# Kernel tuning notes

Measured on AMD Instinct MI355X. Metric: run time of the kernel, lower is better.

The kernel has to match this reference:

```python
import jax, jax.numpy as jnp
import numpy as np

D_MODEL = 1024
HEADS = 16
DH = D_MODEL // HEADS
ROPE_THETA = 10000.0


def _rope_cache(T, dh, base, dtype):
    half = dh // 2
    inv_freq = 1.0 / (base ** (jnp.arange(half, dtype=dtype) / half))
    t = jnp.arange(T, dtype=dtype)
    freqs = jnp.outer(t, inv_freq)  # [T, half]
    return jnp.sin(freqs), jnp.cos(freqs)


def _apply_rope(x, sin, cos):
    # x: [B, h, T, dh]; sin/cos: [T, dh//2] broadcast over B,h
    half = sin.shape[-1]
    x1, x2 = x[..., :half], x[..., half:2 * half]
    return jnp.concatenate([x1 * cos - x2 * sin, x1 * sin + x2 * cos], axis=-1)


def setup_inputs() -> dict:
    key = jax.random.key(0)
    ks = jax.random.split(key, 5)
    B, T, D = 4, 2048, D_MODEL
    scale = 1.0 / np.sqrt(D)
    x_btd = jax.random.normal(ks[0], (B, T, D), dtype=jnp.float32)
    Wqkv = jax.random.normal(ks[1], (D, 3 * D), dtype=jnp.float32) * scale
    bqkv = jnp.zeros((3 * D,), dtype=jnp.float32)
    Wproj = jax.random.normal(ks[2], (D, D), dtype=jnp.float32) * scale
    bproj = jnp.zeros((D,), dtype=jnp.float32)
    return {"x_btd": x_btd, "Wqkv": Wqkv, "bqkv": bqkv, "Wproj": Wproj, "bproj": bproj}


def reference(x_btd, Wqkv, bqkv, Wproj, bproj):
    B, T, D = x_btd.shape
    h, dh = HEADS, DH
    qkv = x_btd @ Wqkv + bqkv                      # [B, T, 3D]
    q, k, v = jnp.split(qkv, 3, axis=-1)

    def to_heads(z):
        return z.reshape(B, T, h, dh).transpose(0, 2, 1, 3)  # [B, h, T, dh]

    qh, kh, vh = to_heads(q), to_heads(k), to_heads(v)
    sin, cos = _rope_cache(T, dh, ROPE_THETA, x_btd.dtype)
    qh = _apply_rope(qh, sin, cos)
    kh = _apply_rope(kh, sin, cos)

    scores = jnp.einsum('bhqd,bhkd->bhqk', qh, kh) / jnp.sqrt(jnp.asarray(dh, x_btd.dtype))
    attn = jax.nn.softmax(scores, axis=-1)
    out = jnp.einsum('bhqk,bhkd->bhqd', attn, vh)  # [B, h, T, dh]
    out = out.transpose(0, 2, 1, 3).reshape(B, T, D)
    return out @ Wproj + bproj
```

## Files before the change

kernel.cpp:

```cpp
#include <hip/hip_runtime.h>
#include <stdint.h>


typedef float  f32x4  __attribute__((ext_vector_type(4)));
typedef float  f32x16 __attribute__((ext_vector_type(16)));
typedef short  s16x8  __attribute__((ext_vector_type(8)));
typedef unsigned int u32x4 __attribute__((ext_vector_type(4)));
typedef unsigned short u16;
typedef unsigned int   u32;

#define LOG2E 1.4426950408889634f

__device__ __forceinline__ u16 f2bf(float f) {
  u32 u = __float_as_uint(f);
  u32 r = (u + 0x7fffu + ((u >> 16) & 1u)) >> 16;
  return (u16)r;
}

__device__ __forceinline__ u32 cvtpk_bf16(float lo, float hi) {
  u32 w;
  asm("v_cvt_pk_bf16_f32 %0, %1, %2" : "=v"(w) : "v"(lo), "v"(hi));
  return w;
}

__device__ __forceinline__ float fexp2(float x) {
  return __builtin_amdgcn_exp2f(x);
}

__device__ __forceinline__ void gload_lds16(const u16* g, u16* l) {
  __builtin_amdgcn_global_load_lds(
      (const __attribute__((address_space(1))) uint32_t*)g,
      (__attribute__((address_space(3))) uint32_t*)l, 16, 0, 0);
}

__global__ void rope_table_kernel(float* __restrict__ rsin, float* __restrict__ rcos) {
  int idx = blockIdx.x * 256 + threadIdx.x;
  int t = idx >> 5, i = idx & 31;
  float invf = 1.0f / powf(10000.0f, (float)i * (1.0f / 32.0f));
  float ang = (float)t * invf;
  rsin[idx] = sinf(ang);
  rcos[idx] = cosf(ang);
}

__global__ void cvt_bf16_kernel(const float* __restrict__ in, u16* __restrict__ out) {
  int i = blockIdx.x * 256 + threadIdx.x;
  const float4* p = reinterpret_cast<const float4*>(in) + (size_t)i * 2;
  float4 a = p[0], b = p[1];
  u32 w0 = (u32)f2bf(a.x) | ((u32)f2bf(a.y) << 16);
  u32 w1 = (u32)f2bf(a.z) | ((u32)f2bf(a.w) << 16);
  u32 w2 = (u32)f2bf(b.x) | ((u32)f2bf(b.y) << 16);
  u32 w3 = (u32)f2bf(b.z) | ((u32)f2bf(b.w) << 16);
  reinterpret_cast<uint4*>(out)[i] = make_uint4(w0, w1, w2, w3);
}

__global__ void transpose_cvt_kernel(const float* __restrict__ W, u16* __restrict__ Wt,
                                     int rows , int cols ) {
  __shared__ float tile[32][33];
  int k0 = blockIdx.y * 32, n0 = blockIdx.x * 32;
  int t = threadIdx.x;
  int c = t & 31, r0 = t >> 5;
  #pragma unroll
  for (int i = 0; i < 4; i++) {
    int r = r0 + i * 8;
    tile[r][c] = W[(size_t)(k0 + r) * cols + n0 + c];
  }
  __syncthreads();
  int kk = t & 31, nn0 = t >> 5;
  #pragma unroll
  for (int i = 0; i < 4; i++) {
    int nn = nn0 + i * 8;
    Wt[(size_t)(n0 + nn) * rows + k0 + kk] = f2bf(tile[kk][nn]);
  }
}

__device__ __forceinline__ void qkv_scatter_frag(
    int wavecol, int rbase, int l15, f32x4* accm ,
    const float* bias, const float* rsin, const float* rcos,
    u16* Qg, u16* Kg, u16* Vtg)
{
  int sec = wavecol >> 10;
  int h = (wavecol & 1023) >> 6;
  if (sec < 2) {
    u16* G = (sec == 0) ? Qg : Kg;
    float qs = (sec == 0) ? 0.125f * LOG2E : 1.0f;
    #pragma unroll
    for (int fc = 0; fc < 2; fc++) {
      int dh = fc * 16 + l15;
      float b1 = bias[wavecol + fc * 16 + l15];
      float b2 = bias[wavecol + fc * 16 + l15 + 32];
      #pragma unroll
      for (int j = 0; j < 4; j++) {
        int grow = rbase + j;
        int bidx = grow >> 11, tt = grow & 2047;
        float sn = rsin[tt * 32 + dh], cs = rcos[tt * 32 + dh];
        float v1 = accm[fc][j] + b1;
        float v2 = accm[fc + 2][j] + b2;
        float lo = (v1 * cs - v2 * sn) * qs;
        float hi = (v1 * sn + v2 * cs) * qs;
        size_t base = ((size_t)(bidx * 16 + h) * 2048 + tt) * 64;
        G[base + dh]      = f2bf(lo);
        G[base + dh + 32] = f2bf(hi);
      }
    }
  } else {
    #pragma unroll
    for (int fc = 0; fc < 4; fc++) {
      int dh = fc * 16 + l15;
      float bb = bias[wavecol + fc * 16 + l15];
      #pragma unroll
      for (int j = 0; j < 4; j++) {
        int grow = rbase + j;
        int bidx = grow >> 11, tt = grow & 2047;
        Vtg[((size_t)(bidx * 16 + h) * 64 + dh) * 2048 + tt] = f2bf(accm[fc][j] + bb);
      }
    }
  }
}

template<int MODE>
__global__ __launch_bounds__(256) void gemm_kernel(
    const u16* __restrict__ A, const u16* __restrict__ Bt,
    const float* __restrict__ bias,
    const float* __restrict__ rsin, const float* __restrict__ rcos,
    u16* __restrict__ Qg, u16* __restrict__ Kg, u16* __restrict__ Vtg,
    float* __restrict__ Cout, int K)
{
  __shared__ alignas(16) u16 As[128][64];
  __shared__ alignas(16) u16 Bs[128][64];
  int tid = threadIdx.x;
  int lane = tid & 63, wid = tid >> 6;
  int wr = wid >> 1, wc = wid & 1;
  int l15 = lane & 15, lg = lane >> 4;
  int row0 = blockIdx.x * 128, col0 = blockIdx.y * 128;

  f32x4 acc[4][4] = {};

  int sr = lane >> 3, sc = lane & 7;
  int scol = (sc ^ sr) * 8;
  const u16* asrc = A  + (size_t)(row0 + wid * 32 + sr) * K + scol;
  const u16* bsrc = Bt + (size_t)(col0 + wid * 32 + sr) * K + scol;
  u16* aLds = &As[0][0] + wid * 2048;
  u16* bLds = &Bs[0][0] + wid * 2048;

  for (int k0 = 0; k0 < K; k0 += 64) {
    #pragma unroll
    for (int i = 0; i < 4; i++) {
      gload_lds16(asrc + (size_t)(i * 8) * K + k0, aLds + i * 512);
      gload_lds16(bsrc + (size_t)(i * 8) * K + k0, bLds + i * 512);
    }
    __syncthreads();
    #pragma unroll
    for (int kk = 0; kk < 2; kk++) {
      s16x8 af[4], bf[4];
      #pragma unroll
      for (int m = 0; m < 4; m++) {
        int row = wr * 64 + m * 16 + l15;
        int slot = (kk * 4 + lg) ^ (l15 & 7);
        af[m] = *reinterpret_cast<const s16x8*>(&As[row][slot * 8]);
      }
      #pragma unroll
      for (int n = 0; n < 4; n++) {
        int row = wc * 64 + n * 16 + l15;
        int slot = (kk * 4 + lg) ^ (l15 & 7);
        bf[n] = *reinterpret_cast<const s16x8*>(&Bs[row][slot * 8]);
      }
      #pragma unroll
      for (int m = 0; m < 4; m++)
        #pragma unroll
        for (int n = 0; n < 4; n++)
          acc[m][n] = __builtin_amdgcn_mfma_f32_16x16x32_bf16(af[m], bf[n], acc[m][n], 0, 0, 0);
    }
    __syncthreads();
  }

  if (MODE == 0) {
    int wavecol = col0 + wc * 64;
    #pragma unroll
    for (int m = 0; m < 4; m++) {
      int rbase = row0 + wr * 64 + m * 16 + lg * 4;
      qkv_scatter_frag(wavecol, rbase, l15, acc[m], bias, rsin, rcos, Qg, Kg, Vtg);
    }
  } else {
    #pragma unroll
    for (int m = 0; m < 4; m++) {
      int grow = row0 + wr * 64 + m * 16 + lg * 4;
      #pragma unroll
      for (int fc = 0; fc < 4; fc++) {
        int col = col0 + wc * 64 + fc * 16 + l15;
        float bb = bias[col];
        #pragma unroll
        for (int j = 0; j < 4; j++)
          Cout[(size_t)(grow + j) * 1024 + col] = acc[m][fc][j] + bb;
      }
    }
  }
}

template<int MODE>
__global__ __launch_bounds__(512, 2) void gemm8_kernel(
    const u16* __restrict__ A, const u16* __restrict__ Bt,
    const float* __restrict__ bias,
    const float* __restrict__ rsin, const float* __restrict__ rcos,
    u16* __restrict__ Qg, u16* __restrict__ Kg, u16* __restrict__ Vtg,
    float* __restrict__ Cout, int K)
{
  extern __shared__ u16 lds[];
  int tid = threadIdx.x;
  int lane = tid & 63, wid = tid >> 6;
  int wr = wid >> 2, wc = wid & 3;
  int l15 = lane & 15, lg = lane >> 4;
  int row0 = blockIdx.x * 128, col0 = blockIdx.y * 256;

  f32x4 acc[4][4] = {};

  int sr = lane >> 3, sc = lane & 7;
  int scol = (sc ^ sr) * 8;
  const u16* asrc = A  + (size_t)(row0 + wid * 16 + sr) * K + scol;
  const u16* bsrc = Bt + (size_t)(col0 + wid * 32 + sr) * K + scol;

  #pragma unroll
  for (int i = 0; i < 2; i++)
    gload_lds16(asrc + (size_t)(i * 8) * K, lds + wid * 1024 + i * 512);
  #pragma unroll
  for (int i = 0; i < 4; i++)
    gload_lds16(bsrc + (size_t)(i * 8) * K, lds + 8192 + wid * 2048 + i * 512);
  #pragma unroll
  for (int i = 0; i < 2; i++)
    gload_lds16(asrc + (size_t)(i * 8) * K + 64, lds + 24576 + wid * 1024 + i * 512);
  #pragma unroll
  for (int i = 0; i < 4; i++)
    gload_lds16(bsrc + (size_t)(i * 8) * K + 64, lds + 24576 + 8192 + wid * 2048 + i * 512);
  asm volatile("s_waitcnt vmcnt(6)");
  __builtin_amdgcn_s_barrier();

  const int nt = K >> 6;
  int cur = 0;
  for (int g = 0; g < nt; ++g) {
    const u16* aB = lds + cur * 24576;
    const u16* bB = aB + 8192;
    int nxt = cur + 2; if (nxt >= 3) nxt -= 3;
    u16* aD = lds + nxt * 24576 + wid * 1024;
    u16* bD = lds + nxt * 24576 + 8192 + wid * 2048;
    size_t kn2 = (size_t)(g + 2) << 6;
    bool pre = (g + 2 < nt);

    s16x8 bf[4];
    #pragma unroll
    for (int p = 0; p < 4; p++) {
      const int kk = p >> 1, mh = p & 1;
      const int slotx = (kk * 4 + lg);
      s16x8 af[2];
      #pragma unroll
      for (int mi = 0; mi < 2; mi++) {
        int row = wr * 64 + (mh * 2 + mi) * 16 + l15;
        int slot = slotx ^ (l15 & 7);
        af[mi] = *reinterpret_cast<const s16x8*>(aB + row * 64 + slot * 8);
      }
      if (mh == 0) {
        #pragma unroll
        for (int n = 0; n < 4; n++) {
          int row = wc * 64 + n * 16 + l15;
          int slot = slotx ^ (l15 & 7);
          bf[n] = *reinterpret_cast<const s16x8*>(bB + row * 64 + slot * 8);
        }
      }
      if (p == 0 && pre) {
        #pragma unroll
        for (int i = 0; i < 2; i++)
          gload_lds16(asrc + (size_t)(i * 8) * K + kn2, aD + i * 512);
        #pragma unroll
        for (int i = 0; i < 4; i++)
          gload_lds16(bsrc + (size_t)(i * 8) * K + kn2, bD + i * 512);
      }
      __builtin_amdgcn_s_barrier();
      __builtin_amdgcn_s_setprio(1);
      #pragma unroll
      for (int mi = 0; mi < 2; mi++)
        #pragma unroll
        for (int n = 0; n < 4; n++)
          acc[mh * 2 + mi][n] =
              __builtin_amdgcn_mfma_f32_16x16x32_bf16(af[mi], bf[n], acc[mh * 2 + mi][n], 0, 0, 0);
      __builtin_amdgcn_s_setprio(0);
      __builtin_amdgcn_s_barrier();
    }
    if (pre) {
      asm volatile("s_waitcnt vmcnt(6)");
      __builtin_amdgcn_s_barrier();
    } else if (g + 1 < nt) {
      asm volatile("s_waitcnt vmcnt(0)");
      __builtin_amdgcn_s_barrier();
    }
    cur += 1; if (cur >= 3) cur -= 3;
  }

  if (MODE == 0) {
    int wavecol = col0 + wc * 64;
    #pragma unroll
    for (int m = 0; m < 4; m++) {
      int rbase = row0 + wr * 64 + m * 16 + lg * 4;
      qkv_scatter_frag(wavecol, rbase, l15, acc[m], bias, rsin, rcos, Qg, Kg, Vtg);
    }
  } else {
    #pragma unroll
    for (int m = 0; m < 4; m++) {
      int grow = row0 + wr * 64 + m * 16 + lg * 4;
      #pragma unroll
      for (int fc = 0; fc < 4; fc++) {
        int col = col0 + wc * 64 + fc * 16 + l15;
        float bb = bias[col];
        #pragma unroll
        for (int j = 0; j < 4; j++)
          Cout[(size_t)(grow + j) * 1024 + col] = acc[m][fc][j] + bb;
      }
    }
  }
}

__global__ __launch_bounds__(256, 4) void attn_kernel(
    const u16* __restrict__ Qg, const u16* __restrict__ Kg, const u16* __restrict__ Vtg,
    u16* __restrict__ Og)
{
  __shared__ alignas(16) u16 Ks[2][4096];
  __shared__ alignas(16) u16 Vs[2][4096];
  int tid = threadIdx.x;
  int lane = tid & 63, wid = tid >> 6;
  int l31 = lane & 31, hi = lane >> 5;
  int bh = blockIdx.x & 63, qt = blockIdx.x >> 6;
  int q = qt * 128 + wid * 32 + l31;
  size_t bh2048 = (size_t)bh * 2048;

  s16x8 aq[4];
  #pragma unroll
  for (int kc = 0; kc < 4; kc++)
    aq[kc] = *reinterpret_cast<const s16x8*>(Qg + (bh2048 + q) * 64 + kc * 16 + hi * 8);

  f32x16 o0 = {}, o1 = {};
  float l_run = 0.f;

  int sr = lane >> 3, sc = lane & 7;
  int scol = (sc ^ sr) * 8;
  const u16* kg0 = Kg  + (bh2048 + wid * 16 + sr) * 64 + scol;
  const u16* kg1 = kg0 + 8 * 64;
  const u16* vg0 = Vtg + ((size_t)bh * 64 + wid * 16 + sr) * 2048 + scol;
  const u16* vg1 = vg0 + 8 * 2048;
  int sdst = wid * 1024;

  int offs[2][4];
  #pragma unroll
  for (int c = 0; c < 2; c++)
    #pragma unroll
    for (int j = 0; j < 4; j++)
      offs[c][j] = (c * 32 + l31) * 64 + (((j * 2 + hi) ^ (l31 & 7)) * 8);

#define STAGE(TT, BUF) do { \
    gload_lds16(kg0 + (size_t)(TT) * 4096, &Ks[BUF][sdst]); \
    gload_lds16(kg1 + (size_t)(TT) * 4096, &Ks[BUF][sdst + 512]); \
    gload_lds16(vg0 + (size_t)(TT) * 64,   &Vs[BUF][sdst]); \
    gload_lds16(vg1 + (size_t)(TT) * 64,   &Vs[BUF][sdst + 512]); \
  } while (0)

#define COMPUTE(B) do { \
    const u16* kb = &Ks[B][0]; \
    const u16* vb = &Vs[B][0]; \
    f32x16 s0 = {}, s1 = {}; \
    __builtin_amdgcn_s_setprio(1); \
    _Pragma("unroll") \
    for (int j = 0; j < 4; j++) { \
      s16x8 kf0 = *reinterpret_cast<const s16x8*>(kb + offs[0][j]); \
      s16x8 kf1 = *reinterpret_cast<const s16x8*>(kb + offs[1][j]); \
      s0 = __builtin_amdgcn_mfma_f32_32x32x16_bf16(kf0, aq[j], s0, 0, 0, 0); \
      s1 = __builtin_amdgcn_mfma_f32_32x32x16_bf16(kf1, aq[j], s1, 0, 0, 0); \
    } \
    __builtin_amdgcn_s_setprio(0); \
    _Pragma("unroll") \
    for (int i = 0; i < 16; i++) { \
      s0[i] = fexp2(s0[i]); \
      s1[i] = fexp2(s1[i]); \
    } \
    float r0 = 0.f, r1 = 0.f, r2 = 0.f, r3 = 0.f; \
    _Pragma("unroll") \
    for (int i = 0; i < 4; i++) { \
      r0 += s0[i] + s0[i + 8]; \
      r1 += s0[i + 4] + s0[i + 12]; \
      r2 += s1[i] + s1[i + 8]; \
      r3 += s1[i + 4] + s1[i + 12]; \
    } \
    float rs = (r0 + r1) + (r2 + r3); \
    rs += __shfl_xor(rs, 32); \
    l_run += rs; \
    s16x8 pf[4]; \
    _Pragma("unroll") \
    for (int ks = 0; ks < 2; ks++) { \
      int rr = ks * 8; \
      u32 a0 = cvtpk_bf16(s0[rr + 0], s0[rr + 1]); \
      u32 b0 = cvtpk_bf16(s0[rr + 4], s0[rr + 5]); \
      u32 a1 = cvtpk_bf16(s0[rr + 2], s0[rr + 3]); \
      u32 b1 = cvtpk_bf16(s0[rr + 6], s0[rr + 7]); \
      asm volatile("v_permlane32_swap_b32 %0, %1" : "+v"(a0), "+v"(b0)); \
      asm volatile("v_permlane32_swap_b32 %0, %1" : "+v"(a1), "+v"(b1)); \
      u32x4 w = {a0, a1, b0, b1}; \
      pf[ks] = __builtin_bit_cast(s16x8, w); \
    } \
    _Pragma("unroll") \
    for (int ks = 0; ks < 2; ks++) { \
      int rr = ks * 8; \
      u32 a0 = cvtpk_bf16(s1[rr + 0], s1[rr + 1]); \
      u32 b0 = cvtpk_bf16(s1[rr + 4], s1[rr + 5]); \
      u32 a1 = cvtpk_bf16(s1[rr + 2], s1[rr + 3]); \
      u32 b1 = cvtpk_bf16(s1[rr + 6], s1[rr + 7]); \
      asm volatile("v_permlane32_swap_b32 %0, %1" : "+v"(a0), "+v"(b0)); \
      asm volatile("v_permlane32_swap_b32 %0, %1" : "+v"(a1), "+v"(b1)); \
      u32x4 w = {a0, a1, b0, b1}; \
      pf[ks + 2] = __builtin_bit_cast(s16x8, w); \
    } \
    __builtin_amdgcn_s_setprio(1); \
    _Pragma("unroll") \
    for (int ks = 0; ks < 4; ks++) { \
      s16x8 vf = *reinterpret_cast<const s16x8*>(vb + offs[0][ks]); \
      o0 = __builtin_amdgcn_mfma_f32_32x32x16_bf16(vf, pf[ks], o0, 0, 0, 0); \
    } \
    _Pragma("unroll") \
    for (int ks = 0; ks < 4; ks++) { \
      s16x8 vf = *reinterpret_cast<const s16x8*>(vb + offs[1][ks]); \
      o1 = __builtin_amdgcn_mfma_f32_32x32x16_bf16(vf, pf[ks], o1, 0, 0, 0); \
    } \
    __builtin_amdgcn_s_setprio(0); \
  } while (0)

  STAGE(0, 0);
  __syncthreads();

  for (int it = 0; it < 16; it++) {
    STAGE(2 * it + 1, 1);
    COMPUTE(0);
    __syncthreads();
    if (it < 15) STAGE(2 * it + 2, 0);
    COMPUTE(1);
    __syncthreads();
  }
#undef STAGE
#undef COMPUTE

  float inv = 1.0f / l_run;
  int b = bh >> 4, h = bh & 15;
  size_t rowbase = ((size_t)b * 2048 + q) * 1024 + h * 64;
  #pragma unroll
  for (int c2 = 0; c2 < 2; c2++) {
    #pragma unroll
    for (int g = 0; g < 4; g++) {
      float e0 = (c2 ? o1[g * 4 + 0] : o0[g * 4 + 0]) * inv;
      float e1 = (c2 ? o1[g * 4 + 1] : o0[g * 4 + 1]) * inv;
      float e2 = (c2 ? o1[g * 4 + 2] : o0[g * 4 + 2]) * inv;
      float e3 = (c2 ? o1[g * 4 + 3] : o0[g * 4 + 3]) * inv;
      u32 w0 = cvtpk_bf16(e0, e1);
      u32 w1 = cvtpk_bf16(e2, e3);
      int d = c2 * 32 + g * 8 + hi * 4;
      uint2 val; val.x = w0; val.y = w1;
      *reinterpret_cast<uint2*>(Og + rowbase + d) = val;
    }
  }
}

extern "C" void kernel_launch(void* const* d_in, const int* in_sizes, int n_in,
                              void* d_out, int out_size, void* d_ws, size_t ws_size,
                              hipStream_t stream) {
  const float* x     = (const float*)d_in[0];
  const float* Wqkv  = (const float*)d_in[1];
  const float* bqkv  = (const float*)d_in[2];
  const float* Wproj = (const float*)d_in[3];
  const float* bproj = (const float*)d_in[4];
  float* out = (float*)d_out;

  char* ws = (char*)d_ws;
  size_t off = 0;
  auto alloc = [&](size_t bytes) {
    void* p = ws + off;
    off += (bytes + 255) & ~(size_t)255;
    return p;
  };
  float* rsin  = (float*)alloc((size_t)2048 * 32 * 4);
  float* rcos  = (float*)alloc((size_t)2048 * 32 * 4);
  u16* xb      = (u16*)alloc((size_t)8192 * 1024 * 2);
  u16* Wqkvt   = (u16*)alloc((size_t)3072 * 1024 * 2);
  u16* Wprojt  = (u16*)alloc((size_t)1024 * 1024 * 2);
  u16* Qg      = (u16*)alloc((size_t)64 * 2048 * 64 * 2);
  u16* Kg      = (u16*)alloc((size_t)64 * 2048 * 64 * 2);
  u16* Vtg     = (u16*)alloc((size_t)64 * 2048 * 64 * 2);
  u16* AOg     = (u16*)alloc((size_t)8192 * 1024 * 2);

  rope_table_kernel<<<256, 256, 0, stream>>>(rsin, rcos);
  cvt_bf16_kernel<<<4096, 256, 0, stream>>>(x, xb);
  transpose_cvt_kernel<<<dim3(96, 32), 256, 0, stream>>>(Wqkv, Wqkvt, 1024, 3072);
  transpose_cvt_kernel<<<dim3(32, 32), 256, 0, stream>>>(Wproj, Wprojt, 1024, 1024);

  hipError_t ok0 = hipFuncSetAttribute(
      reinterpret_cast<const void*>(&gemm8_kernel<0>),
      hipFuncAttributeMaxDynamicSharedMemorySize, 147456);
  hipError_t ok1 = hipFuncSetAttribute(
      reinterpret_cast<const void*>(&gemm8_kernel<1>),
      hipFuncAttributeMaxDynamicSharedMemorySize, 147456);

  if (ok0 == hipSuccess) {
    gemm8_kernel<0><<<dim3(64, 12), 512, 147456, stream>>>(
        xb, Wqkvt, bqkv, rsin, rcos, Qg, Kg, Vtg, nullptr, 1024);
  } else {
    gemm_kernel<0><<<dim3(64, 24), 256, 0, stream>>>(
        xb, Wqkvt, bqkv, rsin, rcos, Qg, Kg, Vtg, nullptr, 1024);
  }

  attn_kernel<<<1024, 256, 0, stream>>>(Qg, Kg, Vtg, AOg);

  if (ok1 == hipSuccess) {
    gemm8_kernel<1><<<dim3(64, 4), 512, 147456, stream>>>(
        AOg, Wprojt, bproj, nullptr, nullptr, nullptr, nullptr, nullptr, out, 1024);
  } else {
    gemm_kernel<1><<<dim3(64, 8), 256, 0, stream>>>(
        AOg, Wprojt, bproj, nullptr, nullptr, nullptr, nullptr, nullptr, out, 1024);
  }
}
```

Before: 199.4 us.

## Process two query tiles per wave in attention and merge prep kernels

Each attention wave now handles 64 query rows (two 32-row sub-tiles) instead of 32. K and V fragments read from LDS are shared by both sub-tiles, and the grid is halved to 512 blocks with launch bounds loosened to 2 blocks per CU. Separately, the rope-table, x conversion and two weight transpose kernels are merged into one prep kernel that dispatches on block index, saving three launches. The trade-off is higher register pressure and fewer blocks, which lowers occupancy and latency hiding.

Measured after the change: 258.0 us. 29.4% more time.

```diff
diff --git a/kernel.cpp b/kernel.cpp
--- a/kernel.cpp
+++ b/kernel.cpp
@@ -33,43 +33,54 @@
       (__attribute__((address_space(3))) uint32_t*)l, 16, 0, 0);
 }
 
-__global__ void rope_table_kernel(float* __restrict__ rsin, float* __restrict__ rcos) {
-  int idx = blockIdx.x * 256 + threadIdx.x;
-  int t = idx >> 5, i = idx & 31;
-  float invf = 1.0f / powf(10000.0f, (float)i * (1.0f / 32.0f));
-  float ang = (float)t * invf;
-  rsin[idx] = sinf(ang);
-  rcos[idx] = cosf(ang);
-}
-
-__global__ void cvt_bf16_kernel(const float* __restrict__ in, u16* __restrict__ out) {
-  int i = blockIdx.x * 256 + threadIdx.x;
-  const float4* p = reinterpret_cast<const float4*>(in) + (size_t)i * 2;
-  float4 a = p[0], b = p[1];
-  u32 w0 = (u32)f2bf(a.x) | ((u32)f2bf(a.y) << 16);
-  u32 w1 = (u32)f2bf(a.z) | ((u32)f2bf(a.w) << 16);
-  u32 w2 = (u32)f2bf(b.x) | ((u32)f2bf(b.y) << 16);
-  u32 w3 = (u32)f2bf(b.z) | ((u32)f2bf(b.w) << 16);
-  reinterpret_cast<uint4*>(out)[i] = make_uint4(w0, w1, w2, w3);
-}
-
-__global__ void transpose_cvt_kernel(const float* __restrict__ W, u16* __restrict__ Wt,
-                                     int rows , int cols ) {
-  __shared__ float tile[32][33];
-  int k0 = blockIdx.y * 32, n0 = blockIdx.x * 32;
-  int t = threadIdx.x;
+__device__ __forceinline__ void transpose_body(
+    const float* __restrict__ W, u16* __restrict__ Wt,
+    int rows, int cols, int bx, int by, int t, float* tile )
+{
+  int k0 = by * 32, n0 = bx * 32;
   int c = t & 31, r0 = t >> 5;
   #pragma unroll
   for (int i = 0; i < 4; i++) {
     int r = r0 + i * 8;
-    tile[r][c] = W[(size_t)(k0 + r) * cols + n0 + c];
+    tile[r * 33 + c] = W[(size_t)(k0 + r) * cols + n0 + c];
   }
   __syncthreads();
   int kk = t & 31, nn0 = t >> 5;
   #pragma unroll
   for (int i = 0; i < 4; i++) {
     int nn = nn0 + i * 8;
-    Wt[(size_t)(n0 + nn) * rows + k0 + kk] = f2bf(tile[kk][nn]);
+    Wt[(size_t)(n0 + nn) * rows + k0 + kk] = f2bf(tile[kk * 33 + nn]);
+  }
+}
+
+__global__ void prep_kernel(const float* __restrict__ x, u16* __restrict__ xb,
+                            const float* __restrict__ Wqkv, u16* __restrict__ Wqkvt,
+                            const float* __restrict__ Wproj, u16* __restrict__ Wprojt,
+                            float* __restrict__ rsin, float* __restrict__ rcos) {
+  __shared__ float tile[32 * 33];
+  int bid = blockIdx.x, t = threadIdx.x;
+  if (bid < 4096) {
+    int i = bid * 256 + t;
+    const float4* p = reinterpret_cast<const float4*>(x) + (size_t)i * 2;
+    float4 a = p[0], b = p[1];
+    u32 w0 = (u32)f2bf(a.x) | ((u32)f2bf(a.y) << 16);
+    u32 w1 = (u32)f2bf(a.z) | ((u32)f2bf(a.w) << 16);
+    u32 w2 = (u32)f2bf(b.x) | ((u32)f2bf(b.y) << 16);
+    u32 w3 = (u32)f2bf(b.z) | ((u32)f2bf(b.w) << 16);
+    reinterpret_cast<uint4*>(xb)[i] = make_uint4(w0, w1, w2, w3);
+  } else if (bid < 4096 + 3072) {
+    int bb = bid - 4096;
+    transpose_body(Wqkv, Wqkvt, 1024, 3072, bb % 96, bb / 96, t, tile);
+  } else if (bid < 4096 + 3072 + 1024) {
+    int bb = bid - 7168;
+    transpose_body(Wproj, Wprojt, 1024, 1024, bb % 32, bb / 32, t, tile);
+  } else {
+    int idx = (bid - 8192) * 256 + t;
+    int tt = idx >> 5, i = idx & 31;
+    float invf = 1.0f / powf(10000.0f, (float)i * (1.0f / 32.0f));
+    float ang = (float)tt * invf;
+    rsin[idx] = sinf(ang);
+    rcos[idx] = cosf(ang);
   }
 }
 
@@ -316,7 +327,7 @@
   }
 }
 
-__global__ __launch_bounds__(256, 4) void attn_kernel(
+__global__ __launch_bounds__(256, 2) void attn_kernel(
     const u16* __restrict__ Qg, const u16* __restrict__ Kg, const u16* __restrict__ Vtg,
     u16* __restrict__ Og)
 {
@@ -326,16 +337,18 @@
   int lane = tid & 63, wid = tid >> 6;
   int l31 = lane & 31, hi = lane >> 5;
   int bh = blockIdx.x & 63, qt = blockIdx.x >> 6;
-  int q = qt * 128 + wid * 32 + l31;
+  int q = qt * 256 + wid * 64 + l31;
   size_t bh2048 = (size_t)bh * 2048;
 
-  s16x8 aq[4];
-  #pragma unroll
-  for (int kc = 0; kc < 4; kc++)
-    aq[kc] = *reinterpret_cast<const s16x8*>(Qg + (bh2048 + q) * 64 + kc * 16 + hi * 8);
-
-  f32x16 o0 = {}, o1 = {};
-  float l_run = 0.f;
+  s16x8 aqA[4], aqB[4];
+  #pragma unroll
+  for (int kc = 0; kc < 4; kc++) {
+    aqA[kc] = *reinterpret_cast<const s16x8*>(Qg + (bh2048 + q) * 64 + kc * 16 + hi * 8);
+    aqB[kc] = *reinterpret_cast<const s16x8*>(Qg + (bh2048 + q + 32) * 64 + kc * 16 + hi * 8);
+  }
+
+  f32x16 oA0 = {}, oA1 = {}, oB0 = {}, oB1 = {};
+  float lA = 0.f, lB = 0.f;
 
   int sr = lane >> 3, sc = lane & 7;
   int scol = (sc ^ sr) * 8;
@@ -359,19 +372,7 @@
     gload_lds16(vg1 + (size_t)(TT) * 64,   &Vs[BUF][sdst + 512]); \
   } while (0)
 
-#define COMPUTE(B) do { \
-    const u16* kb = &Ks[B][0]; \
-    const u16* vb = &Vs[B][0]; \
-    f32x16 s0 = {}, s1 = {}; \
-    __builtin_amdgcn_s_setprio(1); \
-    _Pragma("unroll") \
-    for (int j = 0; j < 4; j++) { \
-      s16x8 kf0 = *reinterpret_cast<const s16x8*>(kb + offs[0][j]); \
-      s16x8 kf1 = *reinterpret_cast<const s16x8*>(kb + offs[1][j]); \
-      s0 = __builtin_amdgcn_mfma_f32_32x32x16_bf16(kf0, aq[j], s0, 0, 0, 0); \
-      s1 = __builtin_amdgcn_mfma_f32_32x32x16_bf16(kf1, aq[j], s1, 0, 0, 0); \
-    } \
-    __builtin_amdgcn_s_setprio(0); \
+#define SOFTPACK(s0, s1, lrun, pf) do { \
     _Pragma("unroll") \
     for (int i = 0; i < 16; i++) { \
       s0[i] = fexp2(s0[i]); \
@@ -387,8 +388,7 @@
     } \
     float rs = (r0 + r1) + (r2 + r3); \
     rs += __shfl_xor(rs, 32); \
-    l_run += rs; \
-    s16x8 pf[4]; \
+    lrun += rs; \
     _Pragma("unroll") \
     for (int ks = 0; ks < 2; ks++) { \
       int rr = ks * 8; \
@@ -413,16 +413,42 @@
       u32x4 w = {a0, a1, b0, b1}; \
       pf[ks + 2] = __builtin_bit_cast(s16x8, w); \
     } \
+  } while (0)
+
+#define COMPUTE(B) do { \
+    const u16* kb = &Ks[B][0]; \
+    const u16* vb = &Vs[B][0]; \
+    s16x8 kf[8]; \
+    _Pragma("unroll") \
+    for (int j = 0; j < 4; j++) { \
+      kf[j]     = *reinterpret_cast<const s16x8*>(kb + offs[0][j]); \
+      kf[4 + j] = *reinterpret_cast<const s16x8*>(kb + offs[1][j]); \
+    } \
+    f32x16 sA0 = {}, sA1 = {}, sB0 = {}, sB1 = {}; \
     __builtin_amdgcn_s_setprio(1); \
     _Pragma("unroll") \
+    for (int j = 0; j < 4; j++) { \
+      sA0 = __builtin_amdgcn_mfma_f32_32x32x16_bf16(kf[j],     aqA[j], sA0, 0, 0, 0); \
+      sA1 = __builtin_amdgcn_mfma_f32_32x32x16_bf16(kf[4 + j], aqA[j], sA1, 0, 0, 0); \
+      sB0 = __builtin_amdgcn_mfma_f32_32x32x16_bf16(kf[j],     aqB[j], sB0, 0, 0, 0); \
+      sB1 = __builtin_amdgcn_mfma_f32_32x32x16_bf16(kf[4 + j], aqB[j], sB1, 0, 0, 0); \
+    } \
+    __builtin_amdgcn_s_setprio(0); \
+    s16x8 pfA[4], pfB[4]; \
+    SOFTPACK(sA0, sA1, lA, pfA); \
+    SOFTPACK(sB0, sB1, lB, pfB); \
+    __builtin_amdgcn_s_setprio(1); \
+    _Pragma("unroll") \
     for (int ks = 0; ks < 4; ks++) { \
-      s16x8 vf = *reinterpret_cast<const s16x8*>(vb + offs[0][ks]); \
-      o0 = __builtin_amdgcn_mfma_f32_32x32x16_bf16(vf, pf[ks], o0, 0, 0, 0); \
+      s16x8 vf0 = *reinterpret_cast<const s16x8*>(vb + offs[0][ks]); \
+      oA0 = __builtin_amdgcn_mfma_f32_32x32x16_bf16(vf0, pfA[ks], oA0, 0, 0, 0); \
+      oB0 = __builtin_amdgcn_mfma_f32_32x32x16_bf16(vf0, pfB[ks], oB0, 0, 0, 0); \
     } \
     _Pragma("unroll") \
     for (int ks = 0; ks < 4; ks++) { \
-      s16x8 vf = *reinterpret_cast<const s16x8*>(vb + offs[1][ks]); \
-      o1 = __builtin_amdgcn_mfma_f32_32x32x16_bf16(vf, pf[ks], o1, 0, 0, 0); \
+      s16x8 vf1 = *reinterpret_cast<const s16x8*>(vb + offs[1][ks]); \
+      oA1 = __builtin_amdgcn_mfma_f32_32x32x16_bf16(vf1, pfA[ks], oA1, 0, 0, 0); \
+      oB1 = __builtin_amdgcn_mfma_f32_32x32x16_bf16(vf1, pfB[ks], oB1, 0, 0, 0); \
     } \
     __builtin_amdgcn_s_setprio(0); \
   } while (0)
@@ -440,23 +466,45 @@
   }
 #undef STAGE
 #undef COMPUTE
-
-  float inv = 1.0f / l_run;
+#undef SOFTPACK
+
   int b = bh >> 4, h = bh & 15;
-  size_t rowbase = ((size_t)b * 2048 + q) * 1024 + h * 64;
-  #pragma unroll
-  for (int c2 = 0; c2 < 2; c2++) {
-    #pragma unroll
-    for (int g = 0; g < 4; g++) {
-      float e0 = (c2 ? o1[g * 4 + 0] : o0[g * 4 + 0]) * inv;
-      float e1 = (c2 ? o1[g * 4 + 1] : o0[g * 4 + 1]) * inv;
-      float e2 = (c2 ? o1[g * 4 + 2] : o0[g * 4 + 2]) * inv;
-      float e3 = (c2 ? o1[g * 4 + 3] : o0[g * 4 + 3]) * inv;
-      u32 w0 = cvtpk_bf16(e0, e1);
-      u32 w1 = cvtpk_bf16(e2, e3);
-      int d = c2 * 32 + g * 8 + hi * 4;
-      uint2 val; val.x = w0; val.y = w1;
-      *reinterpret_cast<uint2*>(Og + rowbase + d) = val;
+  {
+    float inv = 1.0f / lA;
+    size_t rowbase = ((size_t)b * 2048 + q) * 1024 + h * 64;
+    #pragma unroll
+    for (int c2 = 0; c2 < 2; c2++) {
+      #pragma unroll
+      for (int g = 0; g < 4; g++) {
+        float e0 = (c2 ? oA1[g * 4 + 0] : oA0[g * 4 + 0]) * inv;
+        float e1 = (c2 ? oA1[g * 4 + 1] : oA0[g * 4 + 1]) * inv;
+        float e2 = (c2 ? oA1[g * 4 + 2] : oA0[g * 4 + 2]) * inv;
+        float e3 = (c2 ? oA1[g * 4 + 3] : oA0[g * 4 + 3]) * inv;
+        u32 w0 = cvtpk_bf16(e0, e1);
+        u32 w1 = cvtpk_bf16(e2, e3);
+        int d = c2 * 32 + g * 8 + hi * 4;
+        uint2 val; val.x = w0; val.y = w1;
+        *reinterpret_cast<uint2*>(Og + rowbase + d) = val;
+      }
+    }
+  }
+  {
+    float inv = 1.0f / lB;
+    size_t rowbase = ((size_t)b * 2048 + q + 32) * 1024 + h * 64;
+    #pragma unroll
+    for (int c2 = 0; c2 < 2; c2++) {
+      #pragma unroll
+      for (int g = 0; g < 4; g++) {
+        float e0 = (c2 ? oB1[g * 4 + 0] : oB0[g * 4 + 0]) * inv;
+        float e1 = (c2 ? oB1[g * 4 + 1] : oB0[g * 4 + 1]) * inv;
+        float e2 = (c2 ? oB1[g * 4 + 2] : oB0[g * 4 + 2]) * inv;
+        float e3 = (c2 ? oB1[g * 4 + 3] : oB0[g * 4 + 3]) * inv;
+        u32 w0 = cvtpk_bf16(e0, e1);
+        u32 w1 = cvtpk_bf16(e2, e3);
+        int d = c2 * 32 + g * 8 + hi * 4;
+        uint2 val; val.x = w0; val.y = w1;
+        *reinterpret_cast<uint2*>(Og + rowbase + d) = val;
+      }
     }
   }
 }
@@ -488,10 +536,7 @@
   u16* Vtg     = (u16*)alloc((size_t)64 * 2048 * 64 * 2);
   u16* AOg     = (u16*)alloc((size_t)8192 * 1024 * 2);
 
-  rope_table_kernel<<<256, 256, 0, stream>>>(rsin, rcos);
-  cvt_bf16_kernel<<<4096, 256, 0, stream>>>(x, xb);
-  transpose_cvt_kernel<<<dim3(96, 32), 256, 0, stream>>>(Wqkv, Wqkvt, 1024, 3072);
-  transpose_cvt_kernel<<<dim3(32, 32), 256, 0, stream>>>(Wproj, Wprojt, 1024, 1024);
+  prep_kernel<<<8448, 256, 0, stream>>>(x, xb, Wqkv, Wqkvt, Wproj, Wprojt, rsin, rcos);
 
   hipError_t ok0 = hipFuncSetAttribute(
       reinterpret_cast<const void*>(&gemm8_kernel<0>),
@@ -508,7 +553,7 @@
         xb, Wqkvt, bqkv, rsin, rcos, Qg, Kg, Vtg, nullptr, 1024);
   }
 
-  attn_kernel<<<1024, 256, 0, stream>>>(Qg, Kg, Vtg, AOg);
+  attn_kernel<<<512, 256, 0, stream>>>(Qg, Kg, Vtg, AOg);
 
   if (ok1 == hipSuccess) {
     gemm8_kernel<1><<<dim3(64, 4), 512, 147456, stream>>>(
```
